# Performance work log

Hardware: AMD Instinct MI355X
Metric: run time of the kernel (lower is better)

Reference implementation:

```python
import jax, jax.numpy as jnp
import numpy as np

L, H, P = 16384, 1024, 512  # seq_len, features, state size


def setup_inputs() -> dict:
    key = jax.random.key(0)
    ks = jax.random.split(key, 7)
    input_sequence = jax.random.normal(ks[0], (L, H), dtype=jnp.float32)
    # Stable diagonal state matrix: real part strictly negative (left half plane)
    Lambda_re = -0.5 * jax.random.uniform(ks[1], (P,), dtype=jnp.float32) - 1e-2
    Lambda_im = 3.0 * jax.random.normal(ks[2], (P,), dtype=jnp.float32)
    # B_tilde = B_ri[...,0] + 1j*B_ri[...,1], shape (P, H); lecun-ish scale
    B_ri = jax.random.normal(ks[3], (P, H, 2), dtype=jnp.float32) / np.sqrt(H)
    # bidirectional: C_tilde has 2P columns (concat of C1, C2)
    C_ri = jax.random.normal(ks[4], (H, 2 * P, 2), dtype=jnp.float32) / np.sqrt(2 * P)
    D = jax.random.normal(ks[5], (H,), dtype=jnp.float32)
    log_step = jax.random.uniform(ks[6], (P,), dtype=jnp.float32,
                                  minval=np.log(1e-3).astype(np.float32),
                                  maxval=np.log(1e-1).astype(np.float32))
    return dict(input_sequence=input_sequence, Lambda_re=Lambda_re,
                Lambda_im=Lambda_im, B_ri=B_ri, C_ri=C_ri, D=D,
                log_step=log_step)


def _binop(ei, ej):
    # associative operator for diagonal linear recurrence x_t = a_t*x_{t-1} + bu_t
    a_i, bu_i = ei
    a_j, bu_j = ej
    return a_i * a_j, a_j * bu_i + bu_j


def reference(input_sequence, Lambda_re, Lambda_im, B_ri, C_ri, D, log_step):
    u = input_sequence  # (L, H) real
    Lam = Lambda_re + 1j * Lambda_im              # (P,) complex
    B_tilde = B_ri[..., 0] + 1j * B_ri[..., 1]    # (P, H) complex
    C_tilde = C_ri[..., 0] + 1j * C_ri[..., 1]    # (H, 2P) complex
    step = jnp.exp(log_step)                      # (P,), step_rescale = 1.0
    # ZOH discretization
    Lambda_bar = jnp.exp(step * Lam)              # (P,)
    B_bar = ((Lambda_bar - 1.0) / Lam)[:, None] * B_tilde  # (P, H)
    # Bu_t = B_bar @ u_t for all t, vectorized as one GEMM: (L,H)@(H,P) -> (L,P)
    Bu = u.astype(B_bar.dtype) @ B_bar.T          # (L, P) complex
    A = jnp.broadcast_to(Lambda_bar, (u.shape[0], Lam.shape[0]))  # (L, P)
    _, xs_f = jax.lax.associative_scan(_binop, (A, Bu))
    _, xs_b = jax.lax.associative_scan(_binop, (A, Bu), reverse=True)
    xs = jnp.concatenate([xs_f, xs_b], axis=1)    # (L, 2P) complex
    # conj_sym=True -> output is 2 * Re(C_tilde @ x)
    ys = 2.0 * (xs @ C_tilde.T).real              # (L, H) real
    return ys + D * u
```

## Files before the change

kernel.cpp:

```cpp
#include <hip/hip_runtime.h>
#include <cstdint>
#include <cmath>

#define L_SEQ 16384
#define H_DIM 1024
#define P_DIM 512
#define NCH   256
#define RCH   64

typedef short short4v __attribute__((ext_vector_type(4)));
typedef short short8v __attribute__((ext_vector_type(8)));
typedef float f32x4   __attribute__((ext_vector_type(4)));

__device__ __forceinline__ unsigned short f2bf(float f) {
    unsigned int u = __float_as_uint(f);
    u += 0x7FFFu + ((u >> 16) & 1u);
    return (unsigned short)(u >> 16);
}

#define GLD16(gp, lp) __builtin_amdgcn_global_load_lds( \
    (const __attribute__((address_space(1))) void*)(gp), \
    (__attribute__((address_space(3))) void*)(lp), 16, 0, 0)

#define VMCNT6 asm volatile("s_waitcnt vmcnt(6)" ::: "memory")
#define VMCNT0 asm volatile("s_waitcnt vmcnt(0)" ::: "memory")
#define BARRIER do { asm volatile("" ::: "memory"); \
                     __builtin_amdgcn_s_barrier(); \
                     asm volatile("" ::: "memory"); } while (0)

__device__ __forceinline__ void lam_pow(const float* Lre, const float* Lim,
                                        const float* lstep, int p, float tmul,
                                        float& ar, float& ai) {
    float step = expf(lstep[p]) * tmul;
    float lr = Lre[p], li = Lim[p];
    float mag = expf(step * lr);
    float ang = step * li;
    ar = mag * cosf(ang);
    ai = mag * sinf(ang);
}


__global__ void conv_u(const float* __restrict__ u, short* __restrict__ ub) {
    size_t i = ((size_t)blockIdx.x * 256 + threadIdx.x) * 8;
    const float4* s = (const float4*)(u + i);
    float4 v0 = s[0], v1 = s[1];
    short8v o;
    o[0] = (short)f2bf(v0.x); o[1] = (short)f2bf(v0.y);
    o[2] = (short)f2bf(v0.z); o[3] = (short)f2bf(v0.w);
    o[4] = (short)f2bf(v1.x); o[5] = (short)f2bf(v1.y);
    o[6] = (short)f2bf(v1.z); o[7] = (short)f2bf(v1.w);
    *(short8v*)&ub[i] = o;
}

__global__ void prep_B(const float* __restrict__ B_ri, short* __restrict__ Bcat,
                       const float* Lre, const float* Lim, const float* lstep) {
    int t = blockIdx.x * 256 + threadIdx.x;
    int p  = t >> 8;
    int h4 = (t & 255) << 2;
    float step = expf(lstep[p]);
    float lr = Lre[p], li = Lim[p];
    float mag = expf(step * lr);
    float cr = mag * cosf(step * li) - 1.0f;
    float ci = mag * sinf(step * li);
    float den = lr * lr + li * li;
    float sr = (cr * lr + ci * li) / den;
    float si = (ci * lr - cr * li) / den;
    const float4* src = (const float4*)(B_ri + ((size_t)p * H_DIM + h4) * 2);
    float4 v0 = src[0], v1 = src[1];
    short4v re, im;
    re[0] = (short)f2bf(sr * v0.x - si * v0.y); im[0] = (short)f2bf(sr * v0.y + si * v0.x);
    re[1] = (short)f2bf(sr * v0.z - si * v0.w); im[1] = (short)f2bf(sr * v0.w + si * v0.z);
    re[2] = (short)f2bf(sr * v1.x - si * v1.y); im[2] = (short)f2bf(sr * v1.y + si * v1.x);
    re[3] = (short)f2bf(sr * v1.z - si * v1.w); im[3] = (short)f2bf(sr * v1.w + si * v1.z);
    *(short4v*)&Bcat[(size_t)p * H_DIM + h4] = re;
    *(short4v*)&Bcat[(size_t)(p + P_DIM) * H_DIM + h4] = im;
}

__global__ void prep_C(const float* __restrict__ C_ri, short* __restrict__ Ccat) {
    int t = blockIdx.x * 256 + threadIdx.x;
    int h  = t >> 8;
    int c4 = (t & 255) << 2;
    const float4* src = (const float4*)(C_ri + ((size_t)h * 1024 + c4) * 2);
    float4 v0 = src[0], v1 = src[1];
    short4v re, im;
    re[0] = (short)f2bf(2.0f * v0.x); im[0] = (short)f2bf(-2.0f * v0.y);
    re[1] = (short)f2bf(2.0f * v0.z); im[1] = (short)f2bf(-2.0f * v0.w);
    re[2] = (short)f2bf(2.0f * v1.x); im[2] = (short)f2bf(-2.0f * v1.y);
    re[3] = (short)f2bf(2.0f * v1.z); im[3] = (short)f2bf(-2.0f * v1.w);
    *(short4v*)&Ccat[(size_t)h * 2048 + c4] = re;
    *(short4v*)&Ccat[(size_t)h * 2048 + 1024 + c4] = im;
}


__global__ void scan_phase_a(const float* __restrict__ Bu, float* __restrict__ E,
                             const float* Lre, const float* Lim, const float* lstep) {
    int chunk = blockIdx.x, dir = blockIdx.y;
    int j = threadIdx.x;
    float ar, ai; lam_pow(Lre, Lim, lstep, j, 1.0f, ar, ai);
    float xr = 0.f, xi = 0.f;
    int base = chunk * RCH;
    for (int i = 0; i < RCH; ++i) {
        int row = dir ? (base + RCH - 1 - i) : (base + i);
        float br = Bu[(size_t)row * 1024 + j];
        float bi = Bu[(size_t)row * 1024 + P_DIM + j];
        float nr = fmaf(ar, xr, fmaf(-ai, xi, br));
        float ni = fmaf(ar, xi, fmaf( ai, xr, bi));
        xr = nr; xi = ni;
    }
    size_t o = ((size_t)dir * NCH + chunk) * 1024 + j;
    E[o] = xr; E[o + P_DIM] = xi;
}

__global__ void scan_carry(const float* __restrict__ E, float* __restrict__ S,
                           const float* Lre, const float* Lim, const float* lstep) {
    int dir = blockIdx.x;
    int j = threadIdx.x;
    float ar, ai; lam_pow(Lre, Lim, lstep, j, (float)RCH, ar, ai);
    float sr = 0.f, si = 0.f;
    for (int t = 0; t < NCH; ++t) {
        int c = dir ? (NCH - 1 - t) : t;
        size_t o = ((size_t)dir * NCH + c) * 1024 + j;
        S[o] = sr; S[o + P_DIM] = si;
        float er = E[o], ei = E[o + P_DIM];
        float nr = fmaf(ar, sr, fmaf(-ai, si, er));
        float ni = fmaf(ar, si, fmaf( ai, sr, ei));
        sr = nr; si = ni;
    }
}

__global__ void scan_phase_c(const float* __restrict__ Bu, const float* __restrict__ S,
                             short* __restrict__ XS,
                             const float* Lre, const float* Lim, const float* lstep) {
    int chunk = blockIdx.x, dir = blockIdx.y;
    int j = threadIdx.x;
    float ar, ai; lam_pow(Lre, Lim, lstep, j, 1.0f, ar, ai);
    size_t so = ((size_t)dir * NCH + chunk) * 1024 + j;
    float xr = S[so], xi = S[so + P_DIM];
    int base = chunk * RCH;
    int reo = dir ? (P_DIM + j) : j;
    int imo = reo + 1024;
    for (int i = 0; i < RCH; ++i) {
        int row = dir ? (base + RCH - 1 - i) : (base + i);
        float br = Bu[(size_t)row * 1024 + j];
        float bi = Bu[(size_t)row * 1024 + P_DIM + j];
        float nr = fmaf(ar, xr, fmaf(-ai, xi, br));
        float ni = fmaf(ar, xi, fmaf( ai, xr, bi));
        xr = nr; xi = ni;
        XS[(size_t)row * 2048 + reo] = (short)f2bf(xr);
        XS[(size_t)row * 2048 + imo] = (short)f2bf(xi);
    }
}

#define SUB(b,op,kh) (&lds[((((b)*2)+(op))*2+(kh))*8192])

#define LDB4(ptr) do { \
    bf0 = *(const short8v*)&(ptr)[roffB];        \
    bf1 = *(const short8v*)&(ptr)[roffB + 512];  \
    bf2 = *(const short8v*)&(ptr)[roffB + 1024]; \
    bf3 = *(const short8v*)&(ptr)[roffB + 1536]; } while (0)

#define LDA4(ptr, mo) do { \
    af0 = *(const short8v*)&(ptr)[roffA + ((mo)+0)*512]; \
    af1 = *(const short8v*)&(ptr)[roffA + ((mo)+1)*512]; \
    af2 = *(const short8v*)&(ptr)[roffA + ((mo)+2)*512]; \
    af3 = *(const short8v*)&(ptr)[roffA + ((mo)+3)*512]; } while (0)

#define MF4(mi, a) \
    acc[mi][0] = __builtin_amdgcn_mfma_f32_16x16x32_bf16(a, bf0, acc[mi][0], 0,0,0); \
    acc[mi][1] = __builtin_amdgcn_mfma_f32_16x16x32_bf16(a, bf1, acc[mi][1], 0,0,0); \
    acc[mi][2] = __builtin_amdgcn_mfma_f32_16x16x32_bf16(a, bf2, acc[mi][2], 0,0,0); \
    acc[mi][3] = __builtin_amdgcn_mfma_f32_16x16x32_bf16(a, bf3, acc[mi][3], 0,0,0);

#define MFMA16(mb) do { \
    __builtin_amdgcn_s_setprio(1); \
    MF4((mb)+0, af0) MF4((mb)+1, af1) MF4((mb)+2, af2) MF4((mb)+3, af3) \
    __builtin_amdgcn_s_setprio(0); } while (0)

template<int M, int N, int K, bool EPI>
__global__ __launch_bounds__(512, 2) void gemm8p(
    const short* __restrict__ A, const short* __restrict__ Bm, float* __restrict__ Co,
    const float* __restrict__ Dv, const float* __restrict__ U)
{
    __shared__ __align__(16) short lds[65536];
    constexpr int NTN = N / 256;
    constexpr int nwg = (M / 256) * NTN;
    constexpr int NT  = K / 64;
    static_assert(nwg % 8 == 0, "bijective XCD swizzle");

    int tid = threadIdx.x;
    int wave = tid >> 6, lane = tid & 63;
    int bid = blockIdx.x;
    int wg  = (bid & 7) * (nwg / 8) + (bid >> 3);
    int m0 = (wg / NTN) * 256, n0 = (wg % NTN) * 256;
    int wm = (wave >> 2) * 128, wn = (wave & 3) * 64;
    int lr = lane & 15;
    int sA = (lane >> 4) ^ ((lane >> 1) & 3);
    int roffA = (wm + lr) * 32 + sA * 8;
    int roffB = (wn + lr) * 32 + sA * 8;

    const short* Ag = A  + (size_t)m0 * K;
    const short* Bg = Bm + (size_t)n0 * K;

    f32x4 acc[8][4];
#pragma unroll
    for (int m = 0; m < 8; ++m)
#pragma unroll
        for (int n = 0; n < 4; ++n) acc[m][n] = (f32x4){0.f, 0.f, 0.f, 0.f};

    auto STAGE = [&](const short* __restrict__ G, int k0, short* sb) {
#pragma unroll
        for (int j = 0; j < 2; ++j) {
            int sl  = j * 512 + tid;
            int row = sl >> 2;
            int s   = (sl & 3) ^ ((row >> 1) & 3);
            GLD16(G + (size_t)row * K + k0 + s * 8, &sb[sl * 8]);
        }
    };

    STAGE(Ag, 0,  SUB(0,0,0));
    STAGE(Bg, 0,  SUB(0,1,0));
    STAGE(Ag, 32, SUB(0,0,1));
    STAGE(Bg, 32, SUB(0,1,1));

    short8v af0, af1, af2, af3, bf0, bf1, bf2, bf3;

    for (int t = 0; t < NT; ++t) {
        int b = t & 1, nb = b ^ 1;
        int tn = (t + 1 < NT) ? (t + 1) : 0;
        const short* Ab0 = SUB(b,0,0); const short* Bb0 = SUB(b,1,0);
        const short* Ab1 = SUB(b,0,1); const short* Bb1 = SUB(b,1,1);

        STAGE(Ag, tn * 64 + 0, SUB(nb,0,0));
        VMCNT6;
        BARRIER;
        LDB4(Bb0);
        LDA4(Ab0, 0);
        MFMA16(0);
        BARRIER;

        STAGE(Bg, tn * 64 + 0, SUB(nb,1,0));
        LDA4(Ab0, 4);
        BARRIER;
        MFMA16(4);
        BARRIER;

        STAGE(Ag, tn * 64 + 32, SUB(nb,0,1));
        VMCNT6;
        BARRIER;
        LDB4(Bb1);
        LDA4(Ab1, 0);
        MFMA16(0);
        BARRIER;

        STAGE(Bg, tn * 64 + 32, SUB(nb,1,1));
        LDA4(Ab1, 4);
        BARRIER;
        MFMA16(4);
        BARRIER;
    }
    VMCNT0;

    int lr4 = (lane >> 4) * 4;
#pragma unroll
    for (int m = 0; m < 8; ++m)
#pragma unroll
        for (int n = 0; n < 4; ++n) {
            int r = m0 + wm + m * 16 + lr4;
            int c = n0 + wn + n * 16 + lr;
#pragma unroll
            for (int i = 0; i < 4; ++i) {
                float v = acc[m][n][i];
                if constexpr (EPI)
                    v = fmaf(Dv[c], U[(size_t)(r + i) * N + c], v);
                Co[(size_t)(r + i) * N + c] = v;
            }
        }
}


extern "C" void kernel_launch(void* const* d_in, const int* in_sizes, int n_in,
                              void* d_out, int out_size, void* d_ws, size_t ws_size,
                              hipStream_t stream) {
    const float* u     = (const float*)d_in[0];
    const float* Lre   = (const float*)d_in[1];
    const float* Lim   = (const float*)d_in[2];
    const float* B_ri  = (const float*)d_in[3];
    const float* C_ri  = (const float*)d_in[4];
    const float* Dv    = (const float*)d_in[5];
    const float* lstep = (const float*)d_in[6];
    float* out = (float*)d_out;

    char* w = (char*)d_ws;
    short* u_bf = (short*)(w);
    short* XS   = (short*)(w);
    short* Bcat = (short*)(w + (64ull  << 20));
    float* Bu   = (float*)(w + (66ull  << 20));
    short* Ccat = (short*)(w + (130ull << 20));
    float* E    = (float*)(w + (134ull << 20));
    float* Scar = (float*)(w + (136ull << 20));

    conv_u<<<(L_SEQ * H_DIM) / (256 * 8), 256, 0, stream>>>(u, u_bf);
    prep_B<<<(P_DIM * H_DIM) / (256 * 4), 256, 0, stream>>>(B_ri, Bcat, Lre, Lim, lstep);
    prep_C<<<(H_DIM * 1024) / (256 * 4), 256, 0, stream>>>(C_ri, Ccat);

    gemm8p<L_SEQ, 1024, H_DIM, false><<<(L_SEQ / 256) * (1024 / 256), 512, 0, stream>>>(
        u_bf, Bcat, Bu, nullptr, nullptr);

    scan_phase_a<<<dim3(NCH, 2), P_DIM, 0, stream>>>(Bu, E, Lre, Lim, lstep);
    scan_carry<<<2, P_DIM, 0, stream>>>(E, Scar, Lre, Lim, lstep);
    scan_phase_c<<<dim3(NCH, 2), P_DIM, 0, stream>>>(Bu, Scar, XS, Lre, Lim, lstep);

    gemm8p<L_SEQ, H_DIM, 2048, true><<<(L_SEQ / 256) * (H_DIM / 256), 512, 0, stream>>>(
        XS, Ccat, out, Dv, u);
}
```

Before: 315.5 us.

## Split carry scan into three-level hierarchy and restructure GEMM barrier schedule

```diff
diff --git a/kernel.cpp b/kernel.cpp
--- a/kernel.cpp
+++ b/kernel.cpp
@@ -111,20 +111,55 @@
     E[o] = xr; E[o + P_DIM] = xi;
 }
 
-__global__ void scan_carry(const float* __restrict__ E, float* __restrict__ S,
-                           const float* Lre, const float* Lim, const float* lstep) {
-    int dir = blockIdx.x;
-    int j = threadIdx.x;
+__global__ void carry_seg(const float* __restrict__ E, float* __restrict__ G,
+                          const float* Lre, const float* Lim, const float* lstep) {
+    int s = blockIdx.x, dir = blockIdx.y, j = threadIdx.x;
     float ar, ai; lam_pow(Lre, Lim, lstep, j, (float)RCH, ar, ai);
-    float sr = 0.f, si = 0.f;
-    for (int t = 0; t < NCH; ++t) {
-        int c = dir ? (NCH - 1 - t) : t;
+    float gr = 0.f, gi = 0.f;
+    for (int t = 0; t < 16; ++t) {
+        int pos = s * 16 + t;
+        int c = dir ? (NCH - 1 - pos) : pos;
         size_t o = ((size_t)dir * NCH + c) * 1024 + j;
-        S[o] = sr; S[o + P_DIM] = si;
         float er = E[o], ei = E[o + P_DIM];
-        float nr = fmaf(ar, sr, fmaf(-ai, si, er));
-        float ni = fmaf(ar, si, fmaf( ai, sr, ei));
-        sr = nr; si = ni;
+        float nr = fmaf(ar, gr, fmaf(-ai, gi, er));
+        float ni = fmaf(ar, gi, fmaf( ai, gr, ei));
+        gr = nr; gi = ni;
+    }
+    size_t o = ((size_t)dir * 16 + s) * 1024 + j;
+    G[o] = gr; G[o + P_DIM] = gi;
+}
+
+__global__ void carry_mid(const float* __restrict__ G, float* __restrict__ T,
+                          const float* Lre, const float* Lim, const float* lstep) {
+    int dir = blockIdx.x, j = threadIdx.x;
+    float ar, ai; lam_pow(Lre, Lim, lstep, j, (float)(RCH * 16), ar, ai);
+    float tr = 0.f, ti = 0.f;
+    for (int s = 0; s < 16; ++s) {
+        size_t o = ((size_t)dir * 16 + s) * 1024 + j;
+        T[o] = tr; T[o + P_DIM] = ti;
+        float gr = G[o], gi = G[o + P_DIM];
+        float nr = fmaf(ar, tr, fmaf(-ai, ti, gr));
+        float ni = fmaf(ar, ti, fmaf( ai, tr, gi));
+        tr = nr; ti = ni;
+    }
+}
+
+__global__ void carry_exp(const float* __restrict__ E, const float* __restrict__ T,
+                          float* __restrict__ S,
+                          const float* Lre, const float* Lim, const float* lstep) {
+    int s = blockIdx.x, dir = blockIdx.y, j = threadIdx.x;
+    float ar, ai; lam_pow(Lre, Lim, lstep, j, (float)RCH, ar, ai);
+    size_t ot = ((size_t)dir * 16 + s) * 1024 + j;
+    float xr = T[ot], xi = T[ot + P_DIM];
+    for (int t = 0; t < 16; ++t) {
+        int pos = s * 16 + t;
+        int c = dir ? (NCH - 1 - pos) : pos;
+        size_t o = ((size_t)dir * NCH + c) * 1024 + j;
+        S[o] = xr; S[o + P_DIM] = xi;
+        float er = E[o], ei = E[o + P_DIM];
+        float nr = fmaf(ar, xr, fmaf(-ai, xi, er));
+        float ni = fmaf(ar, xi, fmaf( ai, xr, ei));
+        xr = nr; xi = ni;
     }
 }
 
@@ -153,31 +188,31 @@
 
 #define SUB(b,op,kh) (&lds[((((b)*2)+(op))*2+(kh))*8192])
 
-#define LDB4(ptr) do { \
-    bf0 = *(const short8v*)&(ptr)[roffB];        \
-    bf1 = *(const short8v*)&(ptr)[roffB + 512];  \
-    bf2 = *(const short8v*)&(ptr)[roffB + 1024]; \
-    bf3 = *(const short8v*)&(ptr)[roffB + 1536]; } while (0)
-
-#define LDA4(ptr, mo) do { \
-    af0 = *(const short8v*)&(ptr)[roffA + ((mo)+0)*512]; \
-    af1 = *(const short8v*)&(ptr)[roffA + ((mo)+1)*512]; \
-    af2 = *(const short8v*)&(ptr)[roffA + ((mo)+2)*512]; \
-    af3 = *(const short8v*)&(ptr)[roffA + ((mo)+3)*512]; } while (0)
+#define LDB(base) do { const short* _p = (base); \
+    b0 = *(const short8v*)&_p[roffB];        b1 = *(const short8v*)&_p[roffB + 512]; \
+    b2 = *(const short8v*)&_p[roffB + 1024]; b3 = *(const short8v*)&_p[roffB + 1536]; } while (0)
+#define LDAL(base) do { const short* _p = (base); \
+    aL0 = *(const short8v*)&_p[roffA];        aL1 = *(const short8v*)&_p[roffA + 512]; \
+    aL2 = *(const short8v*)&_p[roffA + 1024]; aL3 = *(const short8v*)&_p[roffA + 1536]; } while (0)
+#define LDAH(base) do { const short* _p = (base); \
+    aH0 = *(const short8v*)&_p[roffA + 2048]; aH1 = *(const short8v*)&_p[roffA + 2560]; \
+    aH2 = *(const short8v*)&_p[roffA + 3072]; aH3 = *(const short8v*)&_p[roffA + 3584]; } while (0)
 
 #define MF4(mi, a) \
-    acc[mi][0] = __builtin_amdgcn_mfma_f32_16x16x32_bf16(a, bf0, acc[mi][0], 0,0,0); \
-    acc[mi][1] = __builtin_amdgcn_mfma_f32_16x16x32_bf16(a, bf1, acc[mi][1], 0,0,0); \
-    acc[mi][2] = __builtin_amdgcn_mfma_f32_16x16x32_bf16(a, bf2, acc[mi][2], 0,0,0); \
-    acc[mi][3] = __builtin_amdgcn_mfma_f32_16x16x32_bf16(a, bf3, acc[mi][3], 0,0,0);
-
-#define MFMA16(mb) do { \
-    __builtin_amdgcn_s_setprio(1); \
-    MF4((mb)+0, af0) MF4((mb)+1, af1) MF4((mb)+2, af2) MF4((mb)+3, af3) \
+    acc[mi][0] = __builtin_amdgcn_mfma_f32_16x16x32_bf16(a, b0, acc[mi][0], 0,0,0); \
+    acc[mi][1] = __builtin_amdgcn_mfma_f32_16x16x32_bf16(a, b1, acc[mi][1], 0,0,0); \
+    acc[mi][2] = __builtin_amdgcn_mfma_f32_16x16x32_bf16(a, b2, acc[mi][2], 0,0,0); \
+    acc[mi][3] = __builtin_amdgcn_mfma_f32_16x16x32_bf16(a, b3, acc[mi][3], 0,0,0);
+
+#define MFMA16L do { __builtin_amdgcn_s_setprio(1); \
+    MF4(0, aL0) MF4(1, aL1) MF4(2, aL2) MF4(3, aL3) \
     __builtin_amdgcn_s_setprio(0); } while (0)
+#define MFMA16H do { __builtin_amdgcn_s_setprio(1); \
+    MF4(4, aH0) MF4(5, aH1) MF4(6, aH2) MF4(7, aH3) \
+    __builtin_amdgcn_s_setprio(0); } while (0)
 
 template<int M, int N, int K, bool EPI>
-__global__ __launch_bounds__(512, 2) void gemm8p(
+__global__ __launch_bounds__(512, 2) void gemm2r(
     const short* __restrict__ A, const short* __restrict__ Bm, float* __restrict__ Co,
     const float* __restrict__ Dv, const float* __restrict__ U)
 {
@@ -201,62 +236,49 @@
     const short* Ag = A  + (size_t)m0 * K;
     const short* Bg = Bm + (size_t)n0 * K;
 
+    int sl0 = tid, sl1 = 512 + tid;
+    size_t ga0 = (size_t)(sl0 >> 2) * K + (size_t)((((sl0 & 3) ^ ((sl0 >> 3) & 3))) * 8);
+    size_t ga1 = (size_t)(sl1 >> 2) * K + (size_t)((((sl1 & 3) ^ ((sl1 >> 3) & 3))) * 8);
+    int ld0 = sl0 * 8, ld1 = sl1 * 8;
+
     f32x4 acc[8][4];
 #pragma unroll
     for (int m = 0; m < 8; ++m)
 #pragma unroll
         for (int n = 0; n < 4; ++n) acc[m][n] = (f32x4){0.f, 0.f, 0.f, 0.f};
 
-    auto STAGE = [&](const short* __restrict__ G, int k0, short* sb) {
-#pragma unroll
-        for (int j = 0; j < 2; ++j) {
-            int sl  = j * 512 + tid;
-            int row = sl >> 2;
-            int s   = (sl & 3) ^ ((row >> 1) & 3);
-            GLD16(G + (size_t)row * K + k0 + s * 8, &sb[sl * 8]);
-        }
-    };
+#define STAGE(G, k0, sb) do { short* _s = (sb); \
+        GLD16((G) + ga0 + (k0), &_s[ld0]); \
+        GLD16((G) + ga1 + (k0), &_s[ld1]); } while (0)
 
     STAGE(Ag, 0,  SUB(0,0,0));
     STAGE(Bg, 0,  SUB(0,1,0));
     STAGE(Ag, 32, SUB(0,0,1));
     STAGE(Bg, 32, SUB(0,1,1));
 
-    short8v af0, af1, af2, af3, bf0, bf1, bf2, bf3;
+    short8v aL0, aL1, aL2, aL3, aH0, aH1, aH2, aH3, b0, b1, b2, b3;
 
     for (int t = 0; t < NT; ++t) {
         int b = t & 1, nb = b ^ 1;
-        int tn = (t + 1 < NT) ? (t + 1) : 0;
-        const short* Ab0 = SUB(b,0,0); const short* Bb0 = SUB(b,1,0);
-        const short* Ab1 = SUB(b,0,1); const short* Bb1 = SUB(b,1,1);
-
-        STAGE(Ag, tn * 64 + 0, SUB(nb,0,0));
+        int kn = ((t + 1 < NT) ? (t + 1) : 0) * 64;
+        const short* Ab0 = SUB(b,0,0); const short* Ab1 = SUB(b,0,1);
+        const short* Bb0 = SUB(b,1,0); const short* Bb1 = SUB(b,1,1);
+
+        STAGE(Ag, kn, SUB(nb,0,0));
         VMCNT6;
         BARRIER;
-        LDB4(Bb0);
-        LDA4(Ab0, 0);
-        MFMA16(0);
-        BARRIER;
-
-        STAGE(Bg, tn * 64 + 0, SUB(nb,1,0));
-        LDA4(Ab0, 4);
-        BARRIER;
-        MFMA16(4);
-        BARRIER;
-
-        STAGE(Ag, tn * 64 + 32, SUB(nb,0,1));
+        LDB(Bb0); LDAL(Ab0); LDAH(Ab0);
+        MFMA16L;
+        STAGE(Bg, kn, SUB(nb,1,0));
+        MFMA16H;
+
+        STAGE(Ag, kn + 32, SUB(nb,0,1));
         VMCNT6;
         BARRIER;
-        LDB4(Bb1);
-        LDA4(Ab1, 0);
-        MFMA16(0);
-        BARRIER;
-
-        STAGE(Bg, tn * 64 + 32, SUB(nb,1,1));
-        LDA4(Ab1, 4);
-        BARRIER;
-        MFMA16(4);
-        BARRIER;
+        LDB(Bb1); LDAL(Ab1); LDAH(Ab1);
+        MFMA16L;
+        STAGE(Bg, kn + 32, SUB(nb,1,1));
+        MFMA16H;
     }
     VMCNT0;
 
@@ -275,6 +297,7 @@
                 Co[(size_t)(r + i) * N + c] = v;
             }
         }
+#undef STAGE
 }
 
 
@@ -293,6 +316,8 @@
     char* w = (char*)d_ws;
     short* u_bf = (short*)(w);
     short* XS   = (short*)(w);
+    float* Gseg = (float*)(w + (33ull  << 20));
+    float* Tseg = (float*)(w + (34ull  << 20));
     short* Bcat = (short*)(w + (64ull  << 20));
     float* Bu   = (float*)(w + (66ull  << 20));
     short* Ccat = (short*)(w + (130ull << 20));
@@ -303,13 +328,15 @@
     prep_B<<<(P_DIM * H_DIM) / (256 * 4), 256, 0, stream>>>(B_ri, Bcat, Lre, Lim, lstep);
     prep_C<<<(H_DIM * 1024) / (256 * 4), 256, 0, stream>>>(C_ri, Ccat);
 
-    gemm8p<L_SEQ, 1024, H_DIM, false><<<(L_SEQ / 256) * (1024 / 256), 512, 0, stream>>>(
+    gemm2r<L_SEQ, 1024, H_DIM, false><<<(L_SEQ / 256) * (1024 / 256), 512, 0, stream>>>(
         u_bf, Bcat, Bu, nullptr, nullptr);
 
     scan_phase_a<<<dim3(NCH, 2), P_DIM, 0, stream>>>(Bu, E, Lre, Lim, lstep);
-    scan_carry<<<2, P_DIM, 0, stream>>>(E, Scar, Lre, Lim, lstep);
+    carry_seg<<<dim3(16, 2), P_DIM, 0, stream>>>(E, Gseg, Lre, Lim, lstep);
+    carry_mid<<<2, P_DIM, 0, stream>>>(Gseg, Tseg, Lre, Lim, lstep);
+    carry_exp<<<dim3(16, 2), P_DIM, 0, stream>>>(E, Tseg, Scar, Lre, Lim, lstep);
     scan_phase_c<<<dim3(NCH, 2), P_DIM, 0, stream>>>(Bu, Scar, XS, Lre, Lim, lstep);
 
-    gemm8p<L_SEQ, H_DIM, 2048, true><<<(L_SEQ / 256) * (H_DIM / 256), 512, 0, stream>>>(
+    gemm2r<L_SEQ, H_DIM, 2048, true><<<(L_SEQ / 256) * (H_DIM / 256), 512, 0, stream>>>(
         XS, Ccat, out, Dv, u);
 }
```

Result: faster. 302.3 us (-4.2%).
